# Kernel optimization log

Hardware: AMD Instinct MI355X
Metric: run time of the kernel (lower is better)

Reference implementation:

```python
import jax, jax.numpy as jnp
import numpy as np

B, N, C, H = 4, 1024, 1024, 16
HD = C // H
SCALE = HD ** -0.5


def setup_inputs() -> dict:
    key = jax.random.key(0)
    ks = jax.random.split(key, 6)
    s = 0.02
    return {
        "x": jax.random.normal(ks[0], (B, N, C), jnp.float32),
        "k_in": jax.random.normal(ks[1], (B, N, C), jnp.float32),
        "attn_add": jax.random.uniform(ks[2], (B, N, N), jnp.float32),
        "Wq": jax.random.normal(ks[3], (C, C), jnp.float32) * s,
        "Wkv": jax.random.normal(ks[4], (C, 2 * C), jnp.float32) * s,
        "Wproj": jax.random.normal(ks[5], (C, C), jnp.float32) * s,
        "bproj": jnp.zeros((C,), jnp.float32),
    }


def reference(x, k_in, attn_add, Wq, Wkv, Wproj, bproj):
    b, nx, c = x.shape
    nk = k_in.shape[1]
    # q: [B, H, N_x, HD]
    q = (x @ Wq).reshape(b, nx, H, HD).transpose(0, 2, 1, 3)
    # kv: [B, N_k, 2, H, HD] -> k, v each [B, H, N_k, HD]
    kv = (k_in @ Wkv).reshape(b, nk, 2, H, HD)
    k = kv[:, :, 0].transpose(0, 2, 1, 3)
    v = kv[:, :, 1].transpose(0, 2, 1, 3)
    # scores: [B, H, N_x, N_k]
    attn = jnp.einsum("bhnd,bhmd->bhnm", q, k) * SCALE
    attn = jax.nn.softmax(attn, axis=-1)
    # mask-modulated re-softmax: attn_add [B, N_x, N_k] broadcast over heads
    attn = attn * attn_add[:, None, :, :]
    attn = jax.nn.softmax(attn, axis=-1)
    out = jnp.einsum("bhnm,bhmd->bhnd", attn, v)
    out = out.transpose(0, 2, 1, 3).reshape(b, nx, c)
    return out @ Wproj + bproj
```

## Files before the change

kernel.cpp:

```cpp
#include <hip/hip_runtime.h>
#include <cmath>


#define Bb 4
#define Nn 1024
#define Cc 1024
#define Hh 16
#define HD 64

typedef unsigned short u16;
typedef short bf16x8 __attribute__((ext_vector_type(8)));
typedef float f32x4 __attribute__((ext_vector_type(4)));
typedef unsigned short u16x4 __attribute__((ext_vector_type(4)));
typedef __attribute__((address_space(1))) const void* gptr_t;
typedef __attribute__((address_space(3))) void* lptr_t;

__device__ __forceinline__ u16 f2b(float f) {
  union { float f; unsigned u; } x; x.f = f;
  unsigned u = x.u;
  return (u16)((u + 0x7FFFu + ((u >> 16) & 1u)) >> 16);
}
__device__ __forceinline__ float b2f(u16 h) {
  union { unsigned u; float f; } x; x.u = ((unsigned)h) << 16;
  return x.f;
}

__global__ __launch_bounds__(256) void prep_big(
    const float* __restrict__ x, const float* __restrict__ kin,
    const float* __restrict__ af,
    u16* __restrict__ xh, u16* __restrict__ kinh, u16* __restrict__ ab) {
  int i = blockIdx.x * 256 + threadIdx.x;
  xh[i] = f2b(x[i]);
  kinh[i] = f2b(kin[i]);
  ab[i] = f2b(af[i]);
}

__global__ __launch_bounds__(256) void prep_wt(
    const float* __restrict__ Wq, const float* __restrict__ Wkv,
    const float* __restrict__ Wp,
    u16* __restrict__ WqT, u16* __restrict__ WkvTh, u16* __restrict__ WpTh) {
  __shared__ float tile[64][65];
  int id = blockIdx.x;
  const float* src; int srcld; u16* dh; int ot0, it0;
  if (id < 256)      { src = Wq;  srcld = 1024; dh = WqT;
                       ot0 = (id >> 4) * 64; it0 = (id & 15) * 64; }
  else if (id < 768) { id -= 256; src = Wkv; srcld = 2048; dh = WkvTh;
                       ot0 = (id >> 4) * 64; it0 = (id & 15) * 64; }
  else               { id -= 768; src = Wp;  srcld = 1024; dh = WpTh;
                       ot0 = (id >> 4) * 64; it0 = (id & 15) * 64; }
  const int tr = threadIdx.x >> 4;
  const int tc = (threadIdx.x & 15) * 4;
  #pragma unroll
  for (int rr = 0; rr < 4; ++rr) {
    const int r = rr * 16 + tr;
    f32x4 v = *(const f32x4*)&src[(size_t)(it0 + r) * srcld + ot0 + tc];
    tile[r][tc] = v[0]; tile[r][tc + 1] = v[1];
    tile[r][tc + 2] = v[2]; tile[r][tc + 3] = v[3];
  }
  __syncthreads();
  #pragma unroll
  for (int rr = 0; rr < 4; ++rr) {
    const int o = rr * 16 + tr;
    u16x4 hv;
    #pragma unroll
    for (int j = 0; j < 4; ++j) hv[j] = f2b(tile[tc + j][o]);
    *(u16x4*)(dh + (size_t)(ot0 + o) * 1024 + it0 + tc) = hv;
  }
}

__global__ __launch_bounds__(256) void gemm_q(
    const u16* __restrict__ A, const u16* __restrict__ Bt, u16* __restrict__ dsth) {
  constexpr int K = 1024;
  __shared__ u16 As[64 * 32];
  __shared__ u16 Bs[128 * 32];
  const int tid = threadIdx.x;
  const int wave = tid >> 6, lane = tid & 63;
  const int l15 = lane & 15, l4 = lane >> 4;
  const int m0 = blockIdx.x * 64, n0 = blockIdx.y * 128;
  const int wr = wave >> 1, wc = wave & 1;
  const int srow = tid >> 2, scol = (tid & 3) * 8;
  f32x4 acc[2][4] = {};
  const u16* gA  = A  + (size_t)(m0 + srow) * K + scol;
  const u16* gB0 = Bt + (size_t)(n0 + srow) * K + scol;
  const u16* gB1 = Bt + (size_t)(n0 + 64 + srow) * K + scol;
  for (int kt = 0; kt < K; kt += 32) {
    __syncthreads();
    __builtin_amdgcn_global_load_lds((gptr_t)(gA  + kt), (lptr_t)(As + wave * 512), 16, 0, 0);
    __builtin_amdgcn_global_load_lds((gptr_t)(gB0 + kt), (lptr_t)(Bs + wave * 512), 16, 0, 0);
    __builtin_amdgcn_global_load_lds((gptr_t)(gB1 + kt), (lptr_t)(Bs + 2048 + wave * 512), 16, 0, 0);
    __syncthreads();
    bf16x8 af[2], bf_[4];
    #pragma unroll
    for (int i = 0; i < 2; ++i)
      af[i] = *(const bf16x8*)(As + (wr * 32 + i * 16 + l15) * 32 + l4 * 8);
    #pragma unroll
    for (int i = 0; i < 4; ++i)
      bf_[i] = *(const bf16x8*)(Bs + (wc * 64 + i * 16 + l15) * 32 + l4 * 8);
    #pragma unroll
    for (int mi = 0; mi < 2; ++mi)
      #pragma unroll
      for (int ni = 0; ni < 4; ++ni)
        acc[mi][ni] = __builtin_amdgcn_mfma_f32_16x16x32_bf16(af[mi], bf_[ni], acc[mi][ni], 0, 0, 0);
  }
  #pragma unroll
  for (int mi = 0; mi < 2; ++mi)
    #pragma unroll
    for (int ni = 0; ni < 4; ++ni)
      #pragma unroll
      for (int r = 0; r < 4; ++r) {
        const int grow = m0 + wr * 32 + mi * 16 + l4 * 4 + r;
        const int gcol = n0 + wc * 64 + ni * 16 + l15;
        const int bb = grow >> 10, n = grow & 1023, hh = gcol >> 6, d = gcol & 63;
        dsth[(((size_t)(bb * Hh + hh)) * Nn + n) * HD + d] = f2b(acc[mi][ni][r]);
      }
}

__global__ __launch_bounds__(256) void gemm_kv(
    const u16* __restrict__ Ah, const u16* __restrict__ Bh,
    float* __restrict__ dstf, u16* __restrict__ dsth_k, u16* __restrict__ dsth_v) {
  constexpr int K = 1024;
  __shared__ u16 sAh[64 * 32];
  __shared__ u16 sBh[128 * 32];
  const int tid = threadIdx.x;
  const int wave = tid >> 6, lane = tid & 63;
  const int l15 = lane & 15, l4 = lane >> 4;
  const int m0 = blockIdx.x * 64, n0 = blockIdx.y * 128;
  const int wr = wave >> 1, wc = wave & 1;
  const int srow = tid >> 2, scol = (tid & 3) * 8;
  f32x4 acc[2][4] = {};
  const u16* gAh  = Ah + (size_t)(m0 + srow) * K + scol;
  const u16* gBh0 = Bh + (size_t)(n0 + srow) * K + scol;
  const u16* gBh1 = Bh + (size_t)(n0 + 64 + srow) * K + scol;
  for (int kt = 0; kt < K; kt += 32) {
    __syncthreads();
    __builtin_amdgcn_global_load_lds((gptr_t)(gAh  + kt), (lptr_t)(sAh + wave * 512), 16, 0, 0);
    __builtin_amdgcn_global_load_lds((gptr_t)(gBh0 + kt), (lptr_t)(sBh + wave * 512), 16, 0, 0);
    __builtin_amdgcn_global_load_lds((gptr_t)(gBh1 + kt), (lptr_t)(sBh + 2048 + wave * 512), 16, 0, 0);
    __syncthreads();
    bf16x8 fah[2], fbh[4];
    #pragma unroll
    for (int i = 0; i < 2; ++i)
      fah[i] = *(const bf16x8*)(sAh + (wr * 32 + i * 16 + l15) * 32 + l4 * 8);
    #pragma unroll
    for (int i = 0; i < 4; ++i)
      fbh[i] = *(const bf16x8*)(sBh + (wc * 64 + i * 16 + l15) * 32 + l4 * 8);
    #pragma unroll
    for (int mi = 0; mi < 2; ++mi)
      #pragma unroll
      for (int ni = 0; ni < 4; ++ni)
        acc[mi][ni] = __builtin_amdgcn_mfma_f32_16x16x32_bf16(fah[mi], fbh[ni], acc[mi][ni], 0, 0, 0);
  }
  #pragma unroll
  for (int mi = 0; mi < 2; ++mi)
    #pragma unroll
    for (int ni = 0; ni < 4; ++ni)
      #pragma unroll
      for (int r = 0; r < 4; ++r) {
        const int grow = m0 + wr * 32 + mi * 16 + l4 * 4 + r;
        const int gcol = n0 + wc * 64 + ni * 16 + l15;
        const float v = acc[mi][ni][r];
        const int bb = grow >> 10, n = grow & 1023;
        if (n0 < 1024) {
          const int hh = gcol >> 6, d = gcol & 63;
          dsth_k[(((size_t)(bb * Hh + hh)) * Nn + n) * HD + d] = f2b(v);
        } else {
          const int col = gcol - 1024;
          const int hh = col >> 6, d = col & 63;
          const size_t o = (((size_t)(bb * Hh + hh)) * HD + d) * Nn + n;
          dstf[o] = v;
          dsth_v[o] = f2b(v);
        }
      }
}

__global__ __launch_bounds__(256) void sumv_kernel(const float* __restrict__ vtf,
                                                   float* __restrict__ sv) {
  const int bh = blockIdx.x >> 2, d16 = blockIdx.x & 3;
  const int t = threadIdx.x;
  const int d = d16 * 16 + (t >> 4), part = t & 15;
  const float* src = vtf + ((size_t)bh * HD + d) * Nn + part * 64;
  float s = 0.f;
  #pragma unroll
  for (int i = 0; i < 64; i += 4) {
    f32x4 v = *(const f32x4*)(src + i);
    s += v[0] + v[1] + v[2] + v[3];
  }
  s += __shfl_xor(s, 1, 64);
  s += __shfl_xor(s, 2, 64);
  s += __shfl_xor(s, 4, 64);
  s += __shfl_xor(s, 8, 64);
  if (part == 0) sv[(size_t)bh * HD + d] = s;
}

__global__ __launch_bounds__(256, 3) void attn_kernel(
    const u16* __restrict__ qb, const u16* __restrict__ kb,
    const u16* __restrict__ vtb, const float* __restrict__ sv,
    const u16* __restrict__ ab, u16* __restrict__ aoh) {
  __shared__ u16 pt[32 * 128];
  __shared__ u16 at[32 * 136];
  __shared__ float Lp_lds[4][32];
  __shared__ float Ep_lds[4][32];
  __shared__ float Lred[32];
  __shared__ float Ered[32];

  const int tid = threadIdx.x;
  const int wave = tid >> 6, lane = tid & 63;
  const int l15 = lane & 15, l4 = lane >> 4;
  const int bid = (blockIdx.x & 7) * 256 + (blockIdx.x >> 3);
  const int qt = bid & 31, h = (bid >> 5) & 15, b = bid >> 9;
  const size_t bh = (size_t)(b * Hh + h);
  const u16* qg = qb + (bh * Nn + qt * 32) * HD;
  const u16* kg = kb + bh * Nn * HD;
  const u16* vg = vtb + bh * HD * Nn;
  constexpr float C1 = 0.125f * 1.44269504f;

  bf16x8 qf[2][2];
  #pragma unroll
  for (int t2 = 0; t2 < 2; ++t2)
    #pragma unroll
    for (int ks = 0; ks < 2; ++ks)
      qf[t2][ks] = *(const bf16x8*)(qg + (t2 * 16 + l15) * HD + ks * 32 + l4 * 8);

  const int arow = tid >> 3;
  const int acol = (tid & 7) * 16;
  const u16* agp = ab + ((size_t)(b * Nn + qt * 32 + arow)) * Nn + acol;

  {
    bf16x8 a0 = *(const bf16x8*)agp;
    bf16x8 a1 = *(const bf16x8*)(agp + 8);
    *(bf16x8*)(at + arow * 136 + acol) = a0;
    *(bf16x8*)(at + arow * 136 + acol + 8) = a1;
  }
  const u16* kbase = kg + (size_t)(wave * 32 + l15) * HD + l4 * 8;
  bf16x8 kcur0 = *(const bf16x8*)kbase;
  bf16x8 kcur1 = *(const bf16x8*)(kbase + 32);
  bf16x8 kcur2 = *(const bf16x8*)(kbase + 16 * HD);
  bf16x8 kcur3 = *(const bf16x8*)(kbase + 16 * HD + 32);
  __syncthreads();

  float Lp[2][4] = {};
  float ep[2][4] = {};
  f32x4 oacc[2] = {};

  for (int mt = 0; mt < 8; ++mt) {
    bf16x8 kn0, kn1, kn2, kn3;
    bf16x8 an0, an1;
    if (mt < 7) {
      const u16* kr = kbase + (size_t)(mt + 1) * 128 * HD;
      kn0 = *(const bf16x8*)kr;
      kn1 = *(const bf16x8*)(kr + 32);
      kn2 = *(const bf16x8*)(kr + 16 * HD);
      kn3 = *(const bf16x8*)(kr + 16 * HD + 32);
      an0 = *(const bf16x8*)(agp + (mt + 1) * 128);
      an1 = *(const bf16x8*)(agp + (mt + 1) * 128 + 8);
    }
    bf16x8 vf[4];
    #pragma unroll
    for (int k2 = 0; k2 < 4; ++k2)
      vf[k2] = *(const bf16x8*)(vg + (size_t)(wave * 16 + l15) * Nn + (mt << 7) + k2 * 32 + l4 * 8);

    #pragma unroll
    for (int cf = 0; cf < 2; ++cf) {
      bf16x8 ka  = cf ? kcur2 : kcur0;
      bf16x8 kbv = cf ? kcur3 : kcur1;
      f32x4 s0 = {}, s1 = {};
      s0 = __builtin_amdgcn_mfma_f32_16x16x32_bf16(qf[0][0], ka,  s0, 0, 0, 0);
      s0 = __builtin_amdgcn_mfma_f32_16x16x32_bf16(qf[0][1], kbv, s0, 0, 0, 0);
      s1 = __builtin_amdgcn_mfma_f32_16x16x32_bf16(qf[1][0], ka,  s1, 0, 0, 0);
      s1 = __builtin_amdgcn_mfma_f32_16x16x32_bf16(qf[1][1], kbv, s1, 0, 0, 0);
      const int mloc = wave * 32 + cf * 16 + l15;
      #pragma unroll
      for (int r = 0; r < 4; ++r) {
        const int q0 = l4 * 4 + r;
        const float c0 = __builtin_amdgcn_exp2f(s0[r] * C1);
        const float c1 = __builtin_amdgcn_exp2f(s1[r] * C1);
        Lp[0][r] += c0;
        Lp[1][r] += c1;
        const float a0 = b2f(at[q0 * 136 + mloc]);
        const float a1 = b2f(at[(q0 + 16) * 136 + mloc]);
        const float p0 = c0 * a0;
        const float p1 = c1 * a1;
        ep[0][r] += p0;
        ep[1][r] += p1;
        unsigned dpk;
        asm("v_cvt_pk_bf16_f32 %0, %1, %2" : "=v"(dpk) : "v"(p0), "v"(p1));
        const int col = mloc ^ ((q0 & 7) << 3);
        pt[q0 * 128 + col] = (u16)dpk;
        pt[(q0 + 16) * 128 + col] = (u16)(dpk >> 16);
      }
    }
    kcur0 = kn0; kcur1 = kn1; kcur2 = kn2; kcur3 = kn3;
    __syncthreads();

    if (mt < 7) {
      *(bf16x8*)(at + arow * 136 + acol) = an0;
      *(bf16x8*)(at + arow * 136 + acol + 8) = an1;
    }
    #pragma unroll
    for (int t2 = 0; t2 < 2; ++t2)
      #pragma unroll
      for (int k2 = 0; k2 < 4; ++k2) {
        const int row = t2 * 16 + l15;
        bf16x8 df = *(const bf16x8*)(pt + row * 128 + ((k2 * 32 + l4 * 8) ^ ((row & 7) << 3)));
        oacc[t2] = __builtin_amdgcn_mfma_f32_16x16x32_bf16(df, vf[k2], oacc[t2], 0, 0, 0);
      }
    __syncthreads();
  }

  #pragma unroll
  for (int t2 = 0; t2 < 2; ++t2)
    #pragma unroll
    for (int r = 0; r < 4; ++r) {
      float lv = Lp[t2][r];
      lv += __shfl_xor(lv, 1, 64); lv += __shfl_xor(lv, 2, 64);
      lv += __shfl_xor(lv, 4, 64); lv += __shfl_xor(lv, 8, 64);
      float ev = ep[t2][r];
      ev += __shfl_xor(ev, 1, 64); ev += __shfl_xor(ev, 2, 64);
      ev += __shfl_xor(ev, 4, 64); ev += __shfl_xor(ev, 8, 64);
      if (l15 == 0) {
        Lp_lds[wave][t2 * 16 + l4 * 4 + r] = lv;
        Ep_lds[wave][t2 * 16 + l4 * 4 + r] = ev;
      }
    }
  __syncthreads();
  if (tid < 32) {
    Lred[tid] = 1.0f / (Lp_lds[0][tid] + Lp_lds[1][tid] + Lp_lds[2][tid] + Lp_lds[3][tid]);
    Ered[tid] = Ep_lds[0][tid] + Ep_lds[1][tid] + Ep_lds[2][tid] + Ep_lds[3][tid];
  }
  __syncthreads();

  {
    const int d = wave * 16 + l15;
    const float svd = sv[bh * HD + d];
    #pragma unroll
    for (int t2 = 0; t2 < 2; ++t2)
      #pragma unroll
      for (int r = 0; r < 4; ++r) {
        const int row = t2 * 16 + l4 * 4 + r;
        const float linv = Lred[row];
        const float E = fmaf(linv, Ered[row], 1024.0f);
        const float ov = fmaf(linv, oacc[t2][r], svd) / E;
        const int n = qt * 32 + row;
        aoh[((size_t)b * Nn + n) * Cc + h * HD + d] = f2b(ov);
      }
  }
}

__global__ __launch_bounds__(256) void gemm_proj(
    const u16* __restrict__ Ah, const u16* __restrict__ Bh,
    const float* __restrict__ bias, float* __restrict__ dstf) {
  constexpr int K = 1024;
  __shared__ u16 As[64 * 32];
  __shared__ u16 Bs[128 * 32];
  const int tid = threadIdx.x;
  const int wave = tid >> 6, lane = tid & 63;
  const int l15 = lane & 15, l4 = lane >> 4;
  const int m0 = blockIdx.x * 64, n0 = blockIdx.y * 128;
  const int wr = wave >> 1, wc = wave & 1;
  const int srow = tid >> 2, scol = (tid & 3) * 8;
  f32x4 acc[2][4] = {};
  const u16* gA  = Ah + (size_t)(m0 + srow) * K + scol;
  const u16* gB0 = Bh + (size_t)(n0 + srow) * K + scol;
  const u16* gB1 = Bh + (size_t)(n0 + 64 + srow) * K + scol;
  for (int kt = 0; kt < K; kt += 32) {
    __syncthreads();
    __builtin_amdgcn_global_load_lds((gptr_t)(gA  + kt), (lptr_t)(As + wave * 512), 16, 0, 0);
    __builtin_amdgcn_global_load_lds((gptr_t)(gB0 + kt), (lptr_t)(Bs + wave * 512), 16, 0, 0);
    __builtin_amdgcn_global_load_lds((gptr_t)(gB1 + kt), (lptr_t)(Bs + 2048 + wave * 512), 16, 0, 0);
    __syncthreads();
    bf16x8 af[2], bf_[4];
    #pragma unroll
    for (int i = 0; i < 2; ++i)
      af[i] = *(const bf16x8*)(As + (wr * 32 + i * 16 + l15) * 32 + l4 * 8);
    #pragma unroll
    for (int i = 0; i < 4; ++i)
      bf_[i] = *(const bf16x8*)(Bs + (wc * 64 + i * 16 + l15) * 32 + l4 * 8);
    #pragma unroll
    for (int mi = 0; mi < 2; ++mi)
      #pragma unroll
      for (int ni = 0; ni < 4; ++ni)
        acc[mi][ni] = __builtin_amdgcn_mfma_f32_16x16x32_bf16(af[mi], bf_[ni], acc[mi][ni], 0, 0, 0);
  }
  #pragma unroll
  for (int mi = 0; mi < 2; ++mi)
    #pragma unroll
    for (int ni = 0; ni < 4; ++ni)
      #pragma unroll
      for (int r = 0; r < 4; ++r) {
        const int grow = m0 + wr * 32 + mi * 16 + l4 * 4 + r;
        const int gcol = n0 + wc * 64 + ni * 16 + l15;
        dstf[(size_t)grow * Cc + gcol] = acc[mi][ni][r] + bias[gcol];
      }
}

extern "C" void kernel_launch(void* const* d_in, const int* in_sizes, int n_in,
                              void* d_out, int out_size, void* d_ws, size_t ws_size,
                              hipStream_t stream) {
  (void)in_sizes; (void)n_in; (void)out_size; (void)ws_size;
  const float* x   = (const float*)d_in[0];
  const float* kin = (const float*)d_in[1];
  const float* af  = (const float*)d_in[2];
  const float* Wq  = (const float*)d_in[3];
  const float* Wkv = (const float*)d_in[4];
  const float* Wp  = (const float*)d_in[5];
  const float* bp  = (const float*)d_in[6];
  float* out = (float*)d_out;

  char* w = (char*)d_ws;
  auto take = [&](size_t bytes) { char* p = w; w += (bytes + 255) & ~(size_t)255; return p; };
  u16* WqT    = (u16*)take(2097152);
  u16* WkvTh  = (u16*)take(4194304);
  u16* WpTh   = (u16*)take(2097152);
  u16* xh     = (u16*)take(8388608);
  u16* kinh   = (u16*)take(8388608);
  u16* ab     = (u16*)take(8388608);
  u16* qb     = (u16*)take(8388608);
  u16* kb     = (u16*)take(8388608);
  u16* vtb    = (u16*)take(8388608);
  float* vtf  = (float*)take(16777216);
  float* sv   = (float*)take(16384);
  u16* aoh    = (u16*)take(8388608);

  prep_big<<<dim3(16384), dim3(256), 0, stream>>>(x, kin, af, xh, kinh, ab);
  prep_wt<<<dim3(1024), dim3(256), 0, stream>>>(Wq, Wkv, Wp, WqT, WkvTh, WpTh);

  gemm_q<<<dim3(64, 8), dim3(256), 0, stream>>>(xh, WqT, qb);
  gemm_kv<<<dim3(64, 16), dim3(256), 0, stream>>>(kinh, WkvTh, vtf, kb, vtb);
  sumv_kernel<<<dim3(256), dim3(256), 0, stream>>>(vtf, sv);
  attn_kernel<<<dim3(2048), dim3(256), 0, stream>>>(qb, kb, vtb, sv, ab, aoh);
  gemm_proj<<<dim3(64, 8), dim3(256), 0, stream>>>(aoh, WpTh, bp, out);
}
```

Measured before the change: 178.1 us.

## Transpose attn_add into registers, double-buffer P tile, merge Q and KV GEMMs

The attn_add mask is now converted to bf16 and transposed in the weight-prep kernel, so each attention lane loads its mask values straight into registers instead of staging them through an LDS tile. The P tile is double-buffered, which removes one __syncthreads per key tile. The separate Q and KV projection GEMMs are merged into a single launch with a 24-wide grid. This saves one barrier per tile, the LDS staging and one kernel launch, but the transposed mask loads are narrow 8-byte strided reads per lane.

```diff
diff --git a/kernel.cpp b/kernel.cpp
--- a/kernel.cpp
+++ b/kernel.cpp
@@ -27,27 +27,31 @@
 
 __global__ __launch_bounds__(256) void prep_big(
     const float* __restrict__ x, const float* __restrict__ kin,
-    const float* __restrict__ af,
-    u16* __restrict__ xh, u16* __restrict__ kinh, u16* __restrict__ ab) {
+    u16* __restrict__ xh, u16* __restrict__ kinh) {
   int i = blockIdx.x * 256 + threadIdx.x;
   xh[i] = f2b(x[i]);
   kinh[i] = f2b(kin[i]);
-  ab[i] = f2b(af[i]);
 }
 
 __global__ __launch_bounds__(256) void prep_wt(
     const float* __restrict__ Wq, const float* __restrict__ Wkv,
-    const float* __restrict__ Wp,
-    u16* __restrict__ WqT, u16* __restrict__ WkvTh, u16* __restrict__ WpTh) {
+    const float* __restrict__ Wp, const float* __restrict__ af,
+    u16* __restrict__ WqT, u16* __restrict__ WkvTh, u16* __restrict__ WpTh,
+    u16* __restrict__ abT) {
   __shared__ float tile[64][65];
   int id = blockIdx.x;
   const float* src; int srcld; u16* dh; int ot0, it0;
-  if (id < 256)      { src = Wq;  srcld = 1024; dh = WqT;
-                       ot0 = (id >> 4) * 64; it0 = (id & 15) * 64; }
-  else if (id < 768) { id -= 256; src = Wkv; srcld = 2048; dh = WkvTh;
-                       ot0 = (id >> 4) * 64; it0 = (id & 15) * 64; }
-  else               { id -= 768; src = Wp;  srcld = 1024; dh = WpTh;
-                       ot0 = (id >> 4) * 64; it0 = (id & 15) * 64; }
+  if (id < 256)       { src = Wq;  srcld = 1024; dh = WqT;
+                        ot0 = (id >> 4) * 64; it0 = (id & 15) * 64; }
+  else if (id < 768)  { id -= 256; src = Wkv; srcld = 2048; dh = WkvTh;
+                        ot0 = (id >> 4) * 64; it0 = (id & 15) * 64; }
+  else if (id < 1024) { id -= 768; src = Wp;  srcld = 1024; dh = WpTh;
+                        ot0 = (id >> 4) * 64; it0 = (id & 15) * 64; }
+  else                { id -= 1024;
+                        const int ba = id >> 8; id &= 255;
+                        src = af + (size_t)ba * 1048576; srcld = 1024;
+                        dh = abT + (size_t)ba * 1048576;
+                        ot0 = (id >> 4) * 64; it0 = (id & 15) * 64; }
   const int tr = threadIdx.x >> 4;
   const int tc = (threadIdx.x & 15) * 4;
   #pragma unroll
@@ -68,15 +72,23 @@
   }
 }
 
-__global__ __launch_bounds__(256) void gemm_q(
-    const u16* __restrict__ A, const u16* __restrict__ Bt, u16* __restrict__ dsth) {
+__global__ __launch_bounds__(256) void gemm_qkv(
+    const u16* __restrict__ xh, const u16* __restrict__ kinh,
+    const u16* __restrict__ WqT, const u16* __restrict__ WkvTh,
+    u16* __restrict__ qb, u16* __restrict__ kb, u16* __restrict__ vtb,
+    float* __restrict__ vtf) {
   constexpr int K = 1024;
   __shared__ u16 As[64 * 32];
   __shared__ u16 Bs[128 * 32];
   const int tid = threadIdx.x;
   const int wave = tid >> 6, lane = tid & 63;
   const int l15 = lane & 15, l4 = lane >> 4;
-  const int m0 = blockIdx.x * 64, n0 = blockIdx.y * 128;
+  const int y = blockIdx.y;
+  const bool isq = (y < 8);
+  const u16* A  = isq ? xh : kinh;
+  const u16* Bt = isq ? WqT : WkvTh;
+  const int m0 = blockIdx.x * 64;
+  const int n0 = (isq ? y : (y - 8)) * 128;
   const int wr = wave >> 1, wc = wave & 1;
   const int srow = tid >> 2, scol = (tid & 3) * 8;
   f32x4 acc[2][4] = {};
@@ -110,65 +122,20 @@
       for (int r = 0; r < 4; ++r) {
         const int grow = m0 + wr * 32 + mi * 16 + l4 * 4 + r;
         const int gcol = n0 + wc * 64 + ni * 16 + l15;
-        const int bb = grow >> 10, n = grow & 1023, hh = gcol >> 6, d = gcol & 63;
-        dsth[(((size_t)(bb * Hh + hh)) * Nn + n) * HD + d] = f2b(acc[mi][ni][r]);
-      }
-}
-
-__global__ __launch_bounds__(256) void gemm_kv(
-    const u16* __restrict__ Ah, const u16* __restrict__ Bh,
-    float* __restrict__ dstf, u16* __restrict__ dsth_k, u16* __restrict__ dsth_v) {
-  constexpr int K = 1024;
-  __shared__ u16 sAh[64 * 32];
-  __shared__ u16 sBh[128 * 32];
-  const int tid = threadIdx.x;
-  const int wave = tid >> 6, lane = tid & 63;
-  const int l15 = lane & 15, l4 = lane >> 4;
-  const int m0 = blockIdx.x * 64, n0 = blockIdx.y * 128;
-  const int wr = wave >> 1, wc = wave & 1;
-  const int srow = tid >> 2, scol = (tid & 3) * 8;
-  f32x4 acc[2][4] = {};
-  const u16* gAh  = Ah + (size_t)(m0 + srow) * K + scol;
-  const u16* gBh0 = Bh + (size_t)(n0 + srow) * K + scol;
-  const u16* gBh1 = Bh + (size_t)(n0 + 64 + srow) * K + scol;
-  for (int kt = 0; kt < K; kt += 32) {
-    __syncthreads();
-    __builtin_amdgcn_global_load_lds((gptr_t)(gAh  + kt), (lptr_t)(sAh + wave * 512), 16, 0, 0);
-    __builtin_amdgcn_global_load_lds((gptr_t)(gBh0 + kt), (lptr_t)(sBh + wave * 512), 16, 0, 0);
-    __builtin_amdgcn_global_load_lds((gptr_t)(gBh1 + kt), (lptr_t)(sBh + 2048 + wave * 512), 16, 0, 0);
-    __syncthreads();
-    bf16x8 fah[2], fbh[4];
-    #pragma unroll
-    for (int i = 0; i < 2; ++i)
-      fah[i] = *(const bf16x8*)(sAh + (wr * 32 + i * 16 + l15) * 32 + l4 * 8);
-    #pragma unroll
-    for (int i = 0; i < 4; ++i)
-      fbh[i] = *(const bf16x8*)(sBh + (wc * 64 + i * 16 + l15) * 32 + l4 * 8);
-    #pragma unroll
-    for (int mi = 0; mi < 2; ++mi)
-      #pragma unroll
-      for (int ni = 0; ni < 4; ++ni)
-        acc[mi][ni] = __builtin_amdgcn_mfma_f32_16x16x32_bf16(fah[mi], fbh[ni], acc[mi][ni], 0, 0, 0);
-  }
-  #pragma unroll
-  for (int mi = 0; mi < 2; ++mi)
-    #pragma unroll
-    for (int ni = 0; ni < 4; ++ni)
-      #pragma unroll
-      for (int r = 0; r < 4; ++r) {
-        const int grow = m0 + wr * 32 + mi * 16 + l4 * 4 + r;
-        const int gcol = n0 + wc * 64 + ni * 16 + l15;
+        const int bb = grow >> 10, n = grow & 1023;
         const float v = acc[mi][ni][r];
-        const int bb = grow >> 10, n = grow & 1023;
-        if (n0 < 1024) {
+        if (isq) {
           const int hh = gcol >> 6, d = gcol & 63;
-          dsth_k[(((size_t)(bb * Hh + hh)) * Nn + n) * HD + d] = f2b(v);
+          qb[(((size_t)(bb * Hh + hh)) * Nn + n) * HD + d] = f2b(v);
+        } else if (gcol < 1024) {
+          const int hh = gcol >> 6, d = gcol & 63;
+          kb[(((size_t)(bb * Hh + hh)) * Nn + n) * HD + d] = f2b(v);
         } else {
-          const int col = gcol - 1024;
-          const int hh = col >> 6, d = col & 63;
+          const int cv = gcol - 1024;
+          const int hh = cv >> 6, d = cv & 63;
           const size_t o = (((size_t)(bb * Hh + hh)) * HD + d) * Nn + n;
-          dstf[o] = v;
-          dsth_v[o] = f2b(v);
+          vtf[o] = v;
+          vtb[o] = f2b(v);
         }
       }
 }
@@ -195,9 +162,8 @@
 __global__ __launch_bounds__(256, 3) void attn_kernel(
     const u16* __restrict__ qb, const u16* __restrict__ kb,
     const u16* __restrict__ vtb, const float* __restrict__ sv,
-    const u16* __restrict__ ab, u16* __restrict__ aoh) {
-  __shared__ u16 pt[32 * 128];
-  __shared__ u16 at[32 * 136];
+    const u16* __restrict__ abT, u16* __restrict__ aoh) {
+  __shared__ u16 pt[2][32 * 128];
   __shared__ float Lp_lds[4][32];
   __shared__ float Ep_lds[4][32];
   __shared__ float Lred[32];
@@ -221,38 +187,38 @@
     for (int ks = 0; ks < 2; ++ks)
       qf[t2][ks] = *(const bf16x8*)(qg + (t2 * 16 + l15) * HD + ks * 32 + l4 * 8);
 
-  const int arow = tid >> 3;
-  const int acol = (tid & 7) * 16;
-  const u16* agp = ab + ((size_t)(b * Nn + qt * 32 + arow)) * Nn + acol;
-
-  {
-    bf16x8 a0 = *(const bf16x8*)agp;
-    bf16x8 a1 = *(const bf16x8*)(agp + 8);
-    *(bf16x8*)(at + arow * 136 + acol) = a0;
-    *(bf16x8*)(at + arow * 136 + acol + 8) = a1;
-  }
+  const u16* atp = abT + (size_t)b * 1048576
+                 + (size_t)(wave * 32 + l15) * 1024 + qt * 32 + l4 * 4;
+
   const u16* kbase = kg + (size_t)(wave * 32 + l15) * HD + l4 * 8;
   bf16x8 kcur0 = *(const bf16x8*)kbase;
   bf16x8 kcur1 = *(const bf16x8*)(kbase + 32);
   bf16x8 kcur2 = *(const bf16x8*)(kbase + 16 * HD);
   bf16x8 kcur3 = *(const bf16x8*)(kbase + 16 * HD + 32);
-  __syncthreads();
+  u16x4 ac00 = *(const u16x4*)(atp);
+  u16x4 ac01 = *(const u16x4*)(atp + 16);
+  u16x4 ac10 = *(const u16x4*)(atp + 16 * 1024);
+  u16x4 ac11 = *(const u16x4*)(atp + 16 * 1024 + 16);
 
   float Lp[2][4] = {};
   float ep[2][4] = {};
   f32x4 oacc[2] = {};
 
   for (int mt = 0; mt < 8; ++mt) {
+    u16* pb = pt[mt & 1];
     bf16x8 kn0, kn1, kn2, kn3;
-    bf16x8 an0, an1;
+    u16x4 an00, an01, an10, an11;
     if (mt < 7) {
       const u16* kr = kbase + (size_t)(mt + 1) * 128 * HD;
       kn0 = *(const bf16x8*)kr;
       kn1 = *(const bf16x8*)(kr + 32);
       kn2 = *(const bf16x8*)(kr + 16 * HD);
       kn3 = *(const bf16x8*)(kr + 16 * HD + 32);
-      an0 = *(const bf16x8*)(agp + (mt + 1) * 128);
-      an1 = *(const bf16x8*)(agp + (mt + 1) * 128 + 8);
+      const u16* ar = atp + (size_t)(mt + 1) * 128 * 1024;
+      an00 = *(const u16x4*)(ar);
+      an01 = *(const u16x4*)(ar + 16);
+      an10 = *(const u16x4*)(ar + 16 * 1024);
+      an11 = *(const u16x4*)(ar + 16 * 1024 + 16);
     }
     bf16x8 vf[4];
     #pragma unroll
@@ -263,6 +229,8 @@
     for (int cf = 0; cf < 2; ++cf) {
       bf16x8 ka  = cf ? kcur2 : kcur0;
       bf16x8 kbv = cf ? kcur3 : kcur1;
+      u16x4 a4t0 = cf ? ac10 : ac00;
+      u16x4 a4t1 = cf ? ac11 : ac01;
       f32x4 s0 = {}, s1 = {};
       s0 = __builtin_amdgcn_mfma_f32_16x16x32_bf16(qf[0][0], ka,  s0, 0, 0, 0);
       s0 = __builtin_amdgcn_mfma_f32_16x16x32_bf16(qf[0][1], kbv, s0, 0, 0, 0);
@@ -276,35 +244,29 @@
         const float c1 = __builtin_amdgcn_exp2f(s1[r] * C1);
         Lp[0][r] += c0;
         Lp[1][r] += c1;
-        const float a0 = b2f(at[q0 * 136 + mloc]);
-        const float a1 = b2f(at[(q0 + 16) * 136 + mloc]);
-        const float p0 = c0 * a0;
-        const float p1 = c1 * a1;
+        const float p0 = c0 * b2f(a4t0[r]);
+        const float p1 = c1 * b2f(a4t1[r]);
         ep[0][r] += p0;
         ep[1][r] += p1;
         unsigned dpk;
         asm("v_cvt_pk_bf16_f32 %0, %1, %2" : "=v"(dpk) : "v"(p0), "v"(p1));
         const int col = mloc ^ ((q0 & 7) << 3);
-        pt[q0 * 128 + col] = (u16)dpk;
-        pt[(q0 + 16) * 128 + col] = (u16)(dpk >> 16);
+        pb[q0 * 128 + col] = (u16)dpk;
+        pb[(q0 + 16) * 128 + col] = (u16)(dpk >> 16);
       }
     }
     kcur0 = kn0; kcur1 = kn1; kcur2 = kn2; kcur3 = kn3;
-    __syncthreads();
-
-    if (mt < 7) {
-      *(bf16x8*)(at + arow * 136 + acol) = an0;
-      *(bf16x8*)(at + arow * 136 + acol + 8) = an1;
-    }
+    ac00 = an00; ac01 = an01; ac10 = an10; ac11 = an11;
+    __syncthreads();
+
     #pragma unroll
     for (int t2 = 0; t2 < 2; ++t2)
       #pragma unroll
       for (int k2 = 0; k2 < 4; ++k2) {
         const int row = t2 * 16 + l15;
-        bf16x8 df = *(const bf16x8*)(pt + row * 128 + ((k2 * 32 + l4 * 8) ^ ((row & 7) << 3)));
+        bf16x8 df = *(const bf16x8*)(pb + row * 128 + ((k2 * 32 + l4 * 8) ^ ((row & 7) << 3)));
         oacc[t2] = __builtin_amdgcn_mfma_f32_16x16x32_bf16(df, vf[k2], oacc[t2], 0, 0, 0);
       }
-    __syncthreads();
   }
 
   #pragma unroll
@@ -413,7 +375,7 @@
   u16* WpTh   = (u16*)take(2097152);
   u16* xh     = (u16*)take(8388608);
   u16* kinh   = (u16*)take(8388608);
-  u16* ab     = (u16*)take(8388608);
+  u16* abT    = (u16*)take(8388608);
   u16* qb     = (u16*)take(8388608);
   u16* kb     = (u16*)take(8388608);
   u16* vtb    = (u16*)take(8388608);
@@ -421,12 +383,11 @@
   float* sv   = (float*)take(16384);
   u16* aoh    = (u16*)take(8388608);
 
-  prep_big<<<dim3(16384), dim3(256), 0, stream>>>(x, kin, af, xh, kinh, ab);
-  prep_wt<<<dim3(1024), dim3(256), 0, stream>>>(Wq, Wkv, Wp, WqT, WkvTh, WpTh);
-
-  gemm_q<<<dim3(64, 8), dim3(256), 0, stream>>>(xh, WqT, qb);
-  gemm_kv<<<dim3(64, 16), dim3(256), 0, stream>>>(kinh, WkvTh, vtf, kb, vtb);
+  prep_big<<<dim3(16384), dim3(256), 0, stream>>>(x, kin, xh, kinh);
+  prep_wt<<<dim3(2048), dim3(256), 0, stream>>>(Wq, Wkv, Wp, af, WqT, WkvTh, WpTh, abT);
+
+  gemm_qkv<<<dim3(64, 24), dim3(256), 0, stream>>>(xh, kinh, WqT, WkvTh, qb, kb, vtb, vtf);
   sumv_kernel<<<dim3(256), dim3(256), 0, stream>>>(vtf, sv);
-  attn_kernel<<<dim3(2048), dim3(256), 0, stream>>>(qb, kb, vtb, sv, ab, aoh);
+  attn_kernel<<<dim3(2048), dim3(256), 0, stream>>>(qb, kb, vtb, sv, abT, aoh);
   gemm_proj<<<dim3(64, 8), dim3(256), 0, stream>>>(aoh, WpTh, bp, out);
 }
```

Measured after the change: 198.3 us. +11.3%, slower.
